# Performance work log

Hardware: AMD Instinct MI355X
Metric: run time of the kernel (lower is better)

## Reference

```python
import jax, jax.numpy as jnp
import numpy as np
import math

V = 32000      # vocab_size
CTX = 1025     # context_length (S = CTX-1)
L = 4          # num_layers
D = 1024       # hidden_dim
H = 16         # heads
DH = D // H    # head_dim
FF = 4 * D
B = 2
PAD = 3        # padding_idx / tokenizer.pad_id()


def setup_inputs() -> dict:
    key = jax.random.key(0)
    ks = jax.random.split(key, 16)
    g = lambda k, shape: jax.random.normal(k, shape, dtype=jnp.float32) * 0.02
    text = jax.random.randint(ks[0], (B, CTX), 0, V)
    emb = g(ks[1], (V, D)).at[PAD].set(0.0)   # nn.Embedding with padding_idx=3
    u = g(ks[2], (H, DH))
    v = g(ks[3], (H, DH))
    Wq = g(ks[4], (L, D, D))
    Wk = g(ks[5], (L, D, D))
    Wv = g(ks[6], (L, D, D))
    Wr = g(ks[7], (L, D, D))
    Wfc = g(ks[8], (L, D, D))
    bfc = jnp.zeros((L, D), jnp.float32)
    ln1g = jnp.ones((L, D), jnp.float32); ln1b = jnp.zeros((L, D), jnp.float32)
    ln2g = jnp.ones((L, D), jnp.float32); ln2b = jnp.zeros((L, D), jnp.float32)
    W1 = g(ks[9], (L, D, FF)); b1 = jnp.zeros((L, FF), jnp.float32)
    W2 = g(ks[10], (L, FF, D)); b2 = jnp.zeros((L, D), jnp.float32)
    lnfg = jnp.ones((D,), jnp.float32); lnfb = jnp.zeros((D,), jnp.float32)
    Wlm = g(ks[11], (D, V)); blm = jnp.zeros((V,), jnp.float32)
    return dict(text=text, emb=emb, u=u, v=v, Wq=Wq, Wk=Wk, Wv=Wv, Wr=Wr,
                Wfc=Wfc, bfc=bfc, ln1g=ln1g, ln1b=ln1b, ln2g=ln2g, ln2b=ln2b,
                W1=W1, b1=b1, W2=W2, b2=b2, lnfg=lnfg, lnfb=lnfb, Wlm=Wlm, blm=blm)


def _ln(x, g, b, eps=1e-5):
    m = x.mean(-1, keepdims=True)
    va = ((x - m) ** 2).mean(-1, keepdims=True)
    return (x - m) / jnp.sqrt(va + eps) * g + b


def _rel_shift(x):
    # Transformer-XL relative shift: pad a zero column, reshape, drop first row.
    b, h, s, r = x.shape
    xp = jnp.pad(x, ((0, 0), (0, 0), (0, 0), (1, 0)))     # (b,h,s,r+1)
    xp = xp.reshape(b, h, r + 1, s)
    return xp[:, :, 1:, :].reshape(b, h, s, r)


def _forward(text, emb, u, v, Wq, Wk, Wv, Wr, Wfc, bfc, ln1g, ln1b, ln2g, ln2b,
             W1, b1, W2, b2, lnfg, lnfb, Wlm, blm):
    ip = text[:, :-1]                 # ip_text = text[:, :-1]
    S = ip.shape[1]
    x = emb[ip]                       # (B,S,D)
    # PositionalEmbedding over Transformer-XL positions [S-1 .. 0]
    pos = jnp.arange(S - 1, -1, -1, dtype=jnp.float32)
    inv_freq = 1.0 / (10000.0 ** (jnp.arange(0, D, 2, dtype=jnp.float32) / D))
    sinu = pos[:, None] * inv_freq[None, :]
    rel = jnp.concatenate([jnp.sin(sinu), jnp.cos(sinu)], axis=-1)  # (S,D)
    # get_mask: causal triu OR pad-token rows
    causal = jnp.triu(jnp.ones((S, S), dtype=bool), 1)
    pad = (ip == PAD)
    mask = (pad[:, :, None] | causal[None]) [:, None, :, :]        # (B,1,S,S)
    full_row = mask.all(-1, keepdims=True)                          # fully-masked rows -> NaN-fill 0
    scale = 1.0 / math.sqrt(DH)
    for l in range(L):
        xn = _ln(x, ln1g[l], ln1b[l])
        q = (xn @ Wq[l]).reshape(B, S, H, DH).transpose(0, 2, 1, 3)   # (B,H,S,DH)
        k = (xn @ Wk[l]).reshape(B, S, H, DH).transpose(0, 2, 1, 3)
        vv = (xn @ Wv[l]).reshape(B, S, H, DH).transpose(0, 2, 1, 3)
        r = (rel @ Wr[l]).reshape(S, H, DH).transpose(1, 0, 2)        # (H,S,DH)
        term_AC = jnp.einsum('bhqd,bhkd->bhqk', q + u[None, :, None, :], k)
        term_BD = jnp.einsum('bhqd,hkd->bhqk', q + v[None, :, None, :], r)
        term_BD = _rel_shift(term_BD)
        scores = (term_AC + term_BD) * scale
        scores = jnp.where(mask, -1e30, scores)
        aw = jax.nn.softmax(scores, axis=-1)
        aw = jnp.where(full_row, 0.0, aw)                              # NaN -> 0 masking
        o = jnp.einsum('bhqk,bhkd->bhqd', aw, vv).transpose(0, 2, 1, 3).reshape(B, S, D)
        o = o @ Wfc[l] + bfc[l] + xn                                   # fc(out) + attn-input residual
        x = x + o                                                      # block residual
        h = _ln(x, ln2g[l], ln2b[l])
        f = jax.nn.gelu(h @ W1[l] + b1[l])
        f = jax.nn.gelu(f @ W2[l] + b2[l])
        x = x + f
    xf = _ln(x, lnfg, lnfb)
    return xf @ Wlm + blm                                              # (B,S,V) logits


def reference(text, emb, u, v, Wq, Wk, Wv, Wr, Wfc, bfc, ln1g, ln1b, ln2g, ln2b,
              W1, b1, W2, b2, lnfg, lnfb, Wlm, blm):
    return _forward(text, emb, u, v, Wq, Wk, Wv, Wr, Wfc, bfc, ln1g, ln1b,
                    ln2g, ln2b, W1, b1, W2, b2, lnfg, lnfb, Wlm, blm)
```

## Files before the change

### kernel.cpp

```cpp
#include <hip/hip_runtime.h>
#include <stdint.h>

#define S_ 1024
#define D_ 1024
#define H_ 16
#define DH_ 64
#define FF_ 4096
#define B_ 2
#define V_ 32000
#define CTX_ 1025
#define PAD_ 3

typedef unsigned short u16;
typedef __attribute__((ext_vector_type(8))) short bf16x8;
typedef __attribute__((ext_vector_type(4))) float f32x4;

enum { EPI_BF16 = 0, EPI_QKV = 1, EPI_FC = 2, EPI_GELU_BF16 = 3, EPI_GELU_RES = 4, EPI_BIAS_F32 = 5 };

__device__ __forceinline__ u16 f2bf(float f) {
  unsigned u = __float_as_uint(f);
  return (u16)((u + 0x7FFFu + ((u >> 16) & 1u)) >> 16);
}

__device__ __forceinline__ float gelu_f(float x) {
  float t = tanhf(0.7978845608028654f * (x + 0.044715f * x * x * x));
  return 0.5f * x * (1.0f + t);
}

__device__ __forceinline__ void glds16(const void* g, void* l) {
  __builtin_amdgcn_global_load_lds(
      (const __attribute__((address_space(1))) unsigned int*)g,
      (__attribute__((address_space(3))) unsigned int*)l,
      16, 0, 0);
}

__global__ __launch_bounds__(256) void embed_gather(const int* __restrict__ text,
                                                    const float* __restrict__ emb,
                                                    float* __restrict__ x) {
  int row = blockIdx.x;
  int b = row >> 10, s = row & 1023;
  int id = text[b * CTX_ + s];
  float4 v = ((const float4*)(emb + (size_t)id * D_))[threadIdx.x];
  ((float4*)(x + (size_t)row * D_))[threadIdx.x] = v;
}

__global__ __launch_bounds__(256) void rel_enc(u16* __restrict__ rel) {
  int i = blockIdx.x;
  float pos = (float)(S_ - 1 - i);
  for (int t = threadIdx.x; t < 512; t += 256) {
    float invf = exp2f(-(float)t * (13.287712379549449f / 512.0f));
    float ang = pos * invf;
    rel[(size_t)i * D_ + t] = f2bf(sinf(ang));
    rel[(size_t)i * D_ + 512 + t] = f2bf(cosf(ang));
  }
}

__global__ __launch_bounds__(256) void wconv_t(const float* __restrict__ src,
                                               u16* __restrict__ dst, int K, int N) {
  src += (size_t)blockIdx.z * K * N;
  dst += (size_t)blockIdx.z * K * N;
  __shared__ float tile[32][33];
  int n0 = blockIdx.x * 32, k0 = blockIdx.y * 32;
  for (int idx = threadIdx.x; idx < 1024; idx += 256) {
    int r = idx >> 5, c = idx & 31;
    tile[r][c] = src[(size_t)(k0 + r) * N + n0 + c];
  }
  __syncthreads();
  for (int idx = threadIdx.x; idx < 1024; idx += 256) {
    int r = idx >> 5, c = idx & 31;
    dst[(size_t)(n0 + r) * K + k0 + c] = f2bf(tile[c][r]);
  }
}

__global__ __launch_bounds__(256) void wconv4_k(const float* __restrict__ sq,
                                                const float* __restrict__ sk,
                                                const float* __restrict__ sv,
                                                const float* __restrict__ sf,
                                                u16* __restrict__ dqkv,
                                                u16* __restrict__ dfc) {
  const int z = blockIdx.z;
  const float* src = (z == 0) ? sq : (z == 1) ? sk : (z == 2) ? sv : sf;
  u16* dst = (z < 3) ? dqkv + (size_t)z * 1024 * 1024 : dfc;
  __shared__ float tile[32][33];
  int n0 = blockIdx.x * 32, k0 = blockIdx.y * 32;
  for (int idx = threadIdx.x; idx < 1024; idx += 256) {
    int r = idx >> 5, c = idx & 31;
    tile[r][c] = src[(size_t)(k0 + r) * 1024 + n0 + c];
  }
  __syncthreads();
  for (int idx = threadIdx.x; idx < 1024; idx += 256) {
    int r = idx >> 5, c = idx & 31;
    dst[(size_t)(n0 + r) * 1024 + k0 + c] = f2bf(tile[c][r]);
  }
}

__global__ __launch_bounds__(256) void layernorm_k(const float* __restrict__ x,
                                                   const float* __restrict__ g,
                                                   const float* __restrict__ bb,
                                                   float* __restrict__ outf,
                                                   u16* __restrict__ outb) {
  int row = blockIdx.x, tid = threadIdx.x;
  const float* xr = x + (size_t)row * D_;
  float4 v = ((const float4*)xr)[tid];
  float s = v.x + v.y + v.z + v.w;
  float s2 = v.x * v.x + v.y * v.y + v.z * v.z + v.w * v.w;
  __shared__ float red[8];
#pragma unroll
  for (int off = 32; off > 0; off >>= 1) { s += __shfl_xor(s, off); s2 += __shfl_xor(s2, off); }
  if ((tid & 63) == 0) { red[tid >> 6] = s; red[4 + (tid >> 6)] = s2; }
  __syncthreads();
  s = red[0] + red[1] + red[2] + red[3];
  s2 = red[4] + red[5] + red[6] + red[7];
  float mean = s * (1.0f / D_);
  float var = s2 * (1.0f / D_) - mean * mean;
  float rstd = rsqrtf(var + 1e-5f);
  float4 gv = ((const float4*)g)[tid];
  float4 bv = ((const float4*)bb)[tid];
  float y0 = (v.x - mean) * rstd * gv.x + bv.x;
  float y1 = (v.y - mean) * rstd * gv.y + bv.y;
  float y2 = (v.z - mean) * rstd * gv.z + bv.z;
  float y3 = (v.w - mean) * rstd * gv.w + bv.w;
  if (outf) ((float4*)(outf + (size_t)row * D_))[tid] = make_float4(y0, y1, y2, y3);
  ((ushort4*)(outb + (size_t)row * D_))[tid] = make_ushort4(f2bf(y0), f2bf(y1), f2bf(y2), f2bf(y3));
}

__device__ __forceinline__ void epi_one(int mode, float v, int row, int col, int ldc,
                                        void* C0p, void* C1p, void* C2p, void* C3p,
                                        const float* bias0, const float* bias1,
                                        const float* res0) {
  if (mode == EPI_QKV) {
    int seg = col >> 10, c = col & 1023;
    size_t idx = (size_t)row * 1024 + c;
    if (seg == 0) {
      ((u16*)C0p)[idx] = f2bf(v + bias0[c]);
      ((u16*)C1p)[idx] = f2bf(v + bias1[c]);
    } else if (seg == 1) {
      ((u16*)C2p)[idx] = f2bf(v);
    } else {
      ((u16*)C3p)[idx] = f2bf(v);
    }
    return;
  }
  size_t idx = (size_t)row * ldc + col;
  float b0 = bias0 ? bias0[col] : 0.0f;
  if (mode == EPI_BF16) {
    ((u16*)C0p)[idx] = f2bf(v);
  } else if (mode == EPI_FC) {
    float* C0 = (float*)C0p;
    C0[idx] = C0[idx] + v + b0 + res0[idx];
  } else if (mode == EPI_GELU_BF16) {
    ((u16*)C0p)[idx] = f2bf(gelu_f(v + b0));
  } else if (mode == EPI_GELU_RES) {
    float* C0 = (float*)C0p;
    C0[idx] = C0[idx] + gelu_f(v + b0);
  } else {
    ((float*)C0p)[idx] = v + b0;
  }
}

__global__ __launch_bounds__(256) void gemm_bt(const u16* __restrict__ A,
                                               const u16* __restrict__ Bt,
                                               int M, int N, int K,
                                               void* __restrict__ C0p, void* __restrict__ C1p,
                                               void* __restrict__ C2p, void* __restrict__ C3p,
                                               const float* __restrict__ bias0,
                                               const float* __restrict__ bias1,
                                               const float* __restrict__ res0,
                                               int ldc, int mode) {
  __shared__ u16 lA[128 * 32];
  __shared__ u16 lB[128 * 32];
  const int tid = threadIdx.x;
  const int wave = tid >> 6, lane = tid & 63;
  const int i0 = blockIdx.y * 128, j0 = blockIdx.x * 128;
  const int wm = wave & 1, wn = wave >> 1;
  const int m_lane = lane & 15, quad = lane >> 4;

  f32x4 acc[4][4] = {};

  const u16* Ab = A + (size_t)i0 * K;
  const u16* Bb = Bt + (size_t)j0 * K;
  const int r0 = wave * 32 + (lane >> 2);
  const int cb = (lane & 3) * 8;

  for (int k0 = 0; k0 < K; k0 += 32) {
    glds16(Ab + (size_t)r0 * K + k0 + cb, lA + wave * 1024);
    glds16(Ab + (size_t)(r0 + 16) * K + k0 + cb, lA + wave * 1024 + 512);
    glds16(Bb + (size_t)r0 * K + k0 + cb, lB + wave * 1024);
    glds16(Bb + (size_t)(r0 + 16) * K + k0 + cb, lB + wave * 1024 + 512);
    __syncthreads();
    bf16x8 af[4], bfr[4];
#pragma unroll
    for (int t = 0; t < 4; t++) {
      af[t] = *(const bf16x8*)(lA + (wm * 64 + t * 16 + m_lane) * 32 + quad * 8);
      bfr[t] = *(const bf16x8*)(lB + (wn * 64 + t * 16 + m_lane) * 32 + quad * 8);
    }
#pragma unroll
    for (int mt = 0; mt < 4; mt++)
#pragma unroll
      for (int nt = 0; nt < 4; nt++)
        acc[mt][nt] = __builtin_amdgcn_mfma_f32_16x16x32_bf16(af[mt], bfr[nt], acc[mt][nt], 0, 0, 0);
    __syncthreads();
  }

#pragma unroll
  for (int mt = 0; mt < 4; mt++) {
#pragma unroll
    for (int nt = 0; nt < 4; nt++) {
      int col = j0 + wn * 64 + nt * 16 + m_lane;
#pragma unroll
      for (int r = 0; r < 4; r++) {
        int row = i0 + wm * 64 + mt * 16 + quad * 4 + r;
        epi_one(mode, acc[mt][nt][r], row, col, ldc, C0p, C1p, C2p, C3p, bias0, bias1, res0);
      }
    }
  }
}

__global__ __launch_bounds__(256) void gemm_bt64(const u16* __restrict__ A,
                                                 const u16* __restrict__ Bt,
                                                 int M, int N, int K,
                                                 void* __restrict__ C0p, void* __restrict__ C1p,
                                                 void* __restrict__ C2p, void* __restrict__ C3p,
                                                 const float* __restrict__ bias0,
                                                 const float* __restrict__ bias1,
                                                 const float* __restrict__ res0,
                                                 int ldc, int mode) {
  __shared__ u16 lA[64 * 32];
  __shared__ u16 lB[128 * 32];
  const int tid = threadIdx.x;
  const int wave = tid >> 6, lane = tid & 63;
  const int i0 = blockIdx.y * 64, j0 = blockIdx.x * 128;
  const int m_lane = lane & 15, quad = lane >> 4;

  f32x4 acc[4][2] = {};

  const u16* Ab = A + (size_t)i0 * K;
  const u16* Bb = Bt + (size_t)j0 * K;
  const int rA = wave * 16 + (lane >> 2);
  const int rB = wave * 32 + (lane >> 2);
  const int cb = (lane & 3) * 8;

  for (int k0 = 0; k0 < K; k0 += 32) {
    glds16(Ab + (size_t)rA * K + k0 + cb, lA + wave * 512);
    glds16(Bb + (size_t)rB * K + k0 + cb, lB + wave * 1024);
    glds16(Bb + (size_t)(rB + 16) * K + k0 + cb, lB + wave * 1024 + 512);
    __syncthreads();
    bf16x8 af[4], bfr[2];
#pragma unroll
    for (int t = 0; t < 4; t++)
      af[t] = *(const bf16x8*)(lA + (t * 16 + m_lane) * 32 + quad * 8);
#pragma unroll
    for (int t = 0; t < 2; t++)
      bfr[t] = *(const bf16x8*)(lB + (wave * 32 + t * 16 + m_lane) * 32 + quad * 8);
#pragma unroll
    for (int mt = 0; mt < 4; mt++)
#pragma unroll
      for (int nt = 0; nt < 2; nt++)
        acc[mt][nt] = __builtin_amdgcn_mfma_f32_16x16x32_bf16(af[mt], bfr[nt], acc[mt][nt], 0, 0, 0);
    __syncthreads();
  }

#pragma unroll
  for (int mt = 0; mt < 4; mt++) {
#pragma unroll
    for (int nt = 0; nt < 2; nt++) {
      int col = j0 + wave * 32 + nt * 16 + m_lane;
#pragma unroll
      for (int r = 0; r < 4; r++) {
        int row = i0 + mt * 16 + quad * 4 + r;
        epi_one(mode, acc[mt][nt][r], row, col, ldc, C0p, C1p, C2p, C3p, bias0, bias1, res0);
      }
    }
  }
}

__global__ __launch_bounds__(256) void attn_gemm(const u16* __restrict__ A, int lda,
                                                 const u16* __restrict__ Bt, int ldb,
                                                 float* __restrict__ Cf, u16* __restrict__ Cb,
                                                 int K, int mode) {
  const int ti = blockIdx.x, tj = blockIdx.y, bh = blockIdx.z;
  if (mode == 0 && tj > ti) return;
  if (mode == 1 && ti + tj < 15) return;
  const int b = bh >> 4, h = bh & 15;
  __shared__ u16 lA[64 * 64];
  __shared__ u16 lB[64 * 64];
  const int tid = threadIdx.x, wave = tid >> 6, lane = tid & 63;
  const int m_lane = lane & 15, quad = lane >> 4;
  const int i0 = ti * 64, j0 = tj * 64;

  size_t aoff, boff;
  if (mode == 0)      { aoff = (size_t)b * S_ * D_ + h * DH_; boff = (size_t)b * S_ * D_ + h * DH_; }
  else if (mode == 1) { aoff = (size_t)b * S_ * D_ + h * DH_; boff = (size_t)h * DH_; }
  else                { aoff = (size_t)bh * S_ * S_;          boff = (size_t)bh * DH_ * S_; }
  const u16* Ap = A + aoff + (size_t)i0 * lda;
  const u16* Bp = Bt + boff + (mode == 2 ? (size_t)0 : (size_t)j0 * ldb);

  f32x4 acc[4] = {};
  const int cid0 = wave * 128 + lane, cid1 = cid0 + 64;
  const int ar0 = cid0 >> 3, ac0 = (cid0 & 7) * 8;
  const int ar1 = cid1 >> 3, ac1 = (cid1 & 7) * 8;

  const int Kend = (mode == 2) ? (ti + 1) * 64 : K;
  for (int k0 = 0; k0 < Kend; k0 += 64) {
    glds16(Ap + (size_t)ar0 * lda + k0 + ac0, lA + wave * 1024);
    glds16(Ap + (size_t)ar1 * lda + k0 + ac1, lA + wave * 1024 + 512);
    glds16(Bp + (size_t)ar0 * ldb + k0 + ac0, lB + wave * 1024);
    glds16(Bp + (size_t)ar1 * ldb + k0 + ac1, lB + wave * 1024 + 512);
    __syncthreads();
    bf16x8 a0 = *(const bf16x8*)(lA + (wave * 16 + m_lane) * 64 + quad * 8);
    bf16x8 a1 = *(const bf16x8*)(lA + (wave * 16 + m_lane) * 64 + 32 + quad * 8);
#pragma unroll
    for (int nt = 0; nt < 4; nt++) {
      bf16x8 b0 = *(const bf16x8*)(lB + (nt * 16 + m_lane) * 64 + quad * 8);
      bf16x8 b1 = *(const bf16x8*)(lB + (nt * 16 + m_lane) * 64 + 32 + quad * 8);
      acc[nt] = __builtin_amdgcn_mfma_f32_16x16x32_bf16(a0, b0, acc[nt], 0, 0, 0);
      acc[nt] = __builtin_amdgcn_mfma_f32_16x16x32_bf16(a1, b1, acc[nt], 0, 0, 0);
    }
    __syncthreads();
  }

  if (mode == 0) {
    float* C = Cf + (size_t)bh * S_ * S_;
#pragma unroll
    for (int nt = 0; nt < 4; nt++) {
      int col = j0 + nt * 16 + m_lane;
#pragma unroll
      for (int r = 0; r < 4; r++) {
        int row = i0 + wave * 16 + quad * 4 + r;
        C[(size_t)row * S_ + col] = acc[nt][r];
      }
    }
  } else if (mode == 1) {
    float* C = Cf + (size_t)bh * S_ * S_;
#pragma unroll
    for (int nt = 0; nt < 4; nt++) {
      int t = j0 + nt * 16 + m_lane;
#pragma unroll
      for (int r = 0; r < 4; r++) {
        int row = i0 + wave * 16 + quad * 4 + r;
        int j = row + t - (S_ - 1);
        if (j >= 0) C[(size_t)row * S_ + j] += acc[nt][r];
      }
    }
  } else {
    u16* C = Cb + (size_t)b * S_ * D_ + h * DH_;
#pragma unroll
    for (int nt = 0; nt < 4; nt++) {
      int col = nt * 16 + m_lane;
#pragma unroll
      for (int r = 0; r < 4; r++) {
        int row = i0 + wave * 16 + quad * 4 + r;
        C[(size_t)row * D_ + col] = f2bf(acc[nt][r]);
      }
    }
  }
}

__global__ __launch_bounds__(256) void softmax_k(const float* __restrict__ scores,
                                                 u16* __restrict__ aw,
                                                 const int* __restrict__ text) {
  const int i = blockIdx.x, bh = blockIdx.y, b = bh >> 4;
  const float* s = scores + ((size_t)bh * S_ + i) * S_;
  u16* o = aw + ((size_t)bh * S_ + i) * S_;
  const int tid = threadIdx.x, wave = tid >> 6, lane = tid & 63;
  const int n = i + 1;
  const int jmax = ((i >> 6) + 1) << 6;
  const int j0 = tid * 4;
  if (text[b * CTX_ + i] == PAD_) {
    if (j0 < jmax) ((ushort4*)o)[tid] = make_ushort4(0, 0, 0, 0);
    return;
  }
  const float scale = 0.125f;
  float4 sv = ((const float4*)s)[tid];
  float e0 = (j0 + 0 < n) ? sv.x * scale : -3e38f;
  float e1 = (j0 + 1 < n) ? sv.y * scale : -3e38f;
  float e2 = (j0 + 2 < n) ? sv.z * scale : -3e38f;
  float e3 = (j0 + 3 < n) ? sv.w * scale : -3e38f;
  float mx = fmaxf(fmaxf(e0, e1), fmaxf(e2, e3));
  __shared__ float red[8];
#pragma unroll
  for (int off = 32; off > 0; off >>= 1) mx = fmaxf(mx, __shfl_xor(mx, off));
  if (lane == 0) red[wave] = mx;
  __syncthreads();
  mx = fmaxf(fmaxf(red[0], red[1]), fmaxf(red[2], red[3]));
  float p0 = __expf(e0 - mx);
  float p1 = __expf(e1 - mx);
  float p2 = __expf(e2 - mx);
  float p3 = __expf(e3 - mx);
  float sum = p0 + p1 + p2 + p3;
#pragma unroll
  for (int off = 32; off > 0; off >>= 1) sum += __shfl_xor(sum, off);
  if (lane == 0) red[4 + wave] = sum;
  __syncthreads();
  sum = red[4] + red[5] + red[6] + red[7];
  float inv = 1.0f / sum;
  if (j0 < jmax)
    ((ushort4*)o)[tid] = make_ushort4(f2bf(p0 * inv), f2bf(p1 * inv), f2bf(p2 * inv), f2bf(p3 * inv));
}

__global__ __launch_bounds__(256) void v_transpose(const u16* __restrict__ v,
                                                   u16* __restrict__ vT) {
  int bh = blockIdx.y, b = bh >> 4, h = bh & 15;
  int j0 = blockIdx.x * 64;
  __shared__ u16 tile[64][65];
  for (int idx = threadIdx.x; idx < 4096; idx += 256) {
    int jj = idx >> 6, d = idx & 63;
    tile[jj][d] = v[(size_t)(b * S_ + j0 + jj) * D_ + h * DH_ + d];
  }
  __syncthreads();
  for (int idx = threadIdx.x; idx < 4096; idx += 256) {
    int d = idx >> 6, jj = idx & 63;
    vT[((size_t)bh * DH_ + d) * S_ + j0 + jj] = tile[jj][d];
  }
}

extern "C" void kernel_launch(void* const* d_in, const int* in_sizes, int n_in,
                              void* d_out, int out_size, void* d_ws, size_t ws_size,
                              hipStream_t stream) {
  (void)in_sizes; (void)n_in; (void)out_size;
  const int* text = (const int*)d_in[0];
  const float* emb = (const float*)d_in[1];
  const float* u_in = (const float*)d_in[2];
  const float* v_in = (const float*)d_in[3];
  const float* Wq = (const float*)d_in[4];
  const float* Wk = (const float*)d_in[5];
  const float* Wv = (const float*)d_in[6];
  const float* Wr = (const float*)d_in[7];
  const float* Wfc = (const float*)d_in[8];
  const float* bfc = (const float*)d_in[9];
  const float* ln1g = (const float*)d_in[10];
  const float* ln1b = (const float*)d_in[11];
  const float* ln2g = (const float*)d_in[12];
  const float* ln2b = (const float*)d_in[13];
  const float* W1 = (const float*)d_in[14];
  const float* b1 = (const float*)d_in[15];
  const float* W2 = (const float*)d_in[16];
  const float* b2 = (const float*)d_in[17];
  const float* lnfg = (const float*)d_in[18];
  const float* lnfb = (const float*)d_in[19];
  const float* Wlm = (const float*)d_in[20];
  const float* blm = (const float*)d_in[21];
  float* out = (float*)d_out;

  char* w = (char*)d_ws;
  size_t off = 0;
  auto alloc = [&](size_t bytes) -> void* {
    void* p = w + off;
    off += (bytes + 255) & ~(size_t)255;
    return p;
  };
  float* x      = (float*)alloc(2048ull * 1024 * 4);
  float* xnf    = (float*)alloc(2048ull * 1024 * 4);
  u16* xnb      = (u16*)alloc(2048ull * 1024 * 2);
  u16* relb     = (u16*)alloc(1024ull * 1024 * 2);
  u16* wqkvt    = (u16*)alloc(3072ull * 1024 * 2);
  u16* wrt_all  = (u16*)alloc(4096ull * 1024 * 2);
  u16* wfct     = (u16*)alloc(1024ull * 1024 * 2);
  u16* w1t      = (u16*)alloc(4096ull * 1024 * 2);
  u16* w2t      = (u16*)alloc(4096ull * 1024 * 2);
  u16* wlmt     = (u16*)alloc(32000ull * 1024 * 2);
  u16* qu       = (u16*)alloc(2048ull * 1024 * 2);
  u16* qv       = (u16*)alloc(2048ull * 1024 * 2);
  u16* kk       = (u16*)alloc(2048ull * 1024 * 2);
  u16* vv       = (u16*)alloc(2048ull * 1024 * 2);
  u16* vT       = (u16*)alloc(2048ull * 1024 * 2);
  u16* rb_all   = (u16*)alloc(1024ull * 4096 * 2);
  float* scores = (float*)alloc(32ull * 1024 * 1024 * 4);
  u16* aw       = (u16*)alloc(32ull * 1024 * 1024 * 2);
  u16* o_       = (u16*)alloc(2048ull * 1024 * 2);
  u16* f1       = (u16*)alloc(2048ull * 4096 * 2);
  if (off > ws_size) return;

  dim3 blk(256);
  embed_gather<<<2048, blk, 0, stream>>>(text, emb, x);
  rel_enc<<<1024, blk, 0, stream>>>(relb);
  wconv_t<<<dim3(1000, 32), blk, 0, stream>>>(Wlm, wlmt, 1024, 32000);
  wconv_t<<<dim3(32, 32, 4), blk, 0, stream>>>(Wr, wrt_all, 1024, 1024);
  gemm_bt<<<dim3(32, 8), blk, 0, stream>>>(relb, wrt_all, 1024, 4096, 1024,
                                           rb_all, nullptr, nullptr, nullptr,
                                           nullptr, nullptr, nullptr, 4096, EPI_BF16);

  for (int l = 0; l < 4; l++) {
    const size_t dd = 1048576;
    wconv4_k<<<dim3(32, 32, 4), blk, 0, stream>>>(Wq + l * dd, Wk + l * dd, Wv + l * dd,
                                                  Wfc + l * dd, wqkvt, wfct);
    wconv_t<<<dim3(128, 32), blk, 0, stream>>>(W1 + l * 4ull * dd, w1t, 1024, 4096);
    wconv_t<<<dim3(32, 128), blk, 0, stream>>>(W2 + l * 4ull * dd, w2t, 4096, 1024);

    layernorm_k<<<2048, blk, 0, stream>>>(x, ln1g + l * 1024, ln1b + l * 1024, xnf, xnb);

    gemm_bt<<<dim3(24, 16), blk, 0, stream>>>(xnb, wqkvt, 2048, 3072, 1024,
                                              qu, qv, kk, vv, u_in, v_in, nullptr, 1024, EPI_QKV);
    v_transpose<<<dim3(16, 32), blk, 0, stream>>>(vv, vT);

    attn_gemm<<<dim3(16, 16, 32), blk, 0, stream>>>(qu, 1024, kk, 1024, scores, nullptr, 64, 0);
    attn_gemm<<<dim3(16, 16, 32), blk, 0, stream>>>(qv, 1024, rb_all + (size_t)l * 1024, 4096,
                                                    scores, nullptr, 64, 1);
    softmax_k<<<dim3(1024, 32), blk, 0, stream>>>(scores, aw, text);
    attn_gemm<<<dim3(16, 1, 32), blk, 0, stream>>>(aw, 1024, vT, 1024, nullptr, o_, 1024, 2);

    gemm_bt64<<<dim3(8, 32), blk, 0, stream>>>(o_, wfct, 2048, 1024, 1024,
                                               x, nullptr, nullptr, nullptr,
                                               bfc + l * 1024, nullptr, xnf, 1024, EPI_FC);
    layernorm_k<<<2048, blk, 0, stream>>>(x, ln2g + l * 1024, ln2b + l * 1024, nullptr, xnb);
    gemm_bt<<<dim3(32, 16), blk, 0, stream>>>(xnb, w1t, 2048, 4096, 1024,
                                              f1, nullptr, nullptr, nullptr,
                                              b1 + l * 4096, nullptr, nullptr, 4096, EPI_GELU_BF16);
    gemm_bt64<<<dim3(8, 32), blk, 0, stream>>>(f1, w2t, 2048, 1024, 4096,
                                               x, nullptr, nullptr, nullptr,
                                               b2 + l * 1024, nullptr, nullptr, 1024, EPI_GELU_RES);
  }

  layernorm_k<<<2048, blk, 0, stream>>>(x, lnfg, lnfb, nullptr, xnb);
  gemm_bt<<<dim3(250, 16), blk, 0, stream>>>(xnb, wlmt, 2048, 32000, 1024,
                                             out, nullptr, nullptr, nullptr,
                                             blm, nullptr, nullptr, 32000, EPI_BIAS_F32);
}
```

Measured before the change: 2.420 ms.

## Fuse AC and BD score GEMMs with in-block relative shift over causal tiles

Replaces the two separate attention score launches, the content term and the position term with a later read-modify-write, by one kernel. That kernel launches only the 136 lower-triangular tiles per head, computes both terms in registers, and applies the relative shift through a shared-memory staging of the two needed position tiles. It also adds an XCD-aware workgroup remapping to both GEMM kernels and makes softmax skip loading score entries above the causal block. The fused kernel rounds the position term to bf16 before adding it and reads operands straight from global memory without LDS tiling. Both choices risk some precision and load efficiency.

Measured after the change: 2.349 ms. 3.0% less time.

```diff
diff --git a/kernel.cpp b/kernel.cpp
--- a/kernel.cpp
+++ b/kernel.cpp
@@ -20,6 +20,10 @@
 __device__ __forceinline__ u16 f2bf(float f) {
   unsigned u = __float_as_uint(f);
   return (u16)((u + 0x7FFFu + ((u >> 16) & 1u)) >> 16);
+}
+
+__device__ __forceinline__ float bf2f(u16 v) {
+  return __uint_as_float(((unsigned)v) << 16);
 }
 
 __device__ __forceinline__ float gelu_f(float x) {
@@ -171,7 +175,16 @@
   __shared__ u16 lB[128 * 32];
   const int tid = threadIdx.x;
   const int wave = tid >> 6, lane = tid & 63;
-  const int i0 = blockIdx.y * 128, j0 = blockIdx.x * 128;
+  unsigned gx = gridDim.x, gy = gridDim.y;
+  unsigned nwg = gx * gy;
+  unsigned bx = blockIdx.x, by = blockIdx.y;
+  if ((nwg & 7u) == 0u) {
+    unsigned lin = by * gx + bx;
+    unsigned v = (lin & 7u) * (nwg >> 3) + (lin >> 3);
+    bx = v / gy;
+    by = v - bx * gy;
+  }
+  const int i0 = by * 128, j0 = bx * 128;
   const int wm = wave & 1, wn = wave >> 1;
   const int m_lane = lane & 15, quad = lane >> 4;
 
@@ -229,7 +242,16 @@
   __shared__ u16 lB[128 * 32];
   const int tid = threadIdx.x;
   const int wave = tid >> 6, lane = tid & 63;
-  const int i0 = blockIdx.y * 64, j0 = blockIdx.x * 128;
+  unsigned gx = gridDim.x, gy = gridDim.y;
+  unsigned nwg = gx * gy;
+  unsigned bx = blockIdx.x, by = blockIdx.y;
+  if ((nwg & 7u) == 0u) {
+    unsigned lin = by * gx + bx;
+    unsigned v = (lin & 7u) * (nwg >> 3) + (lin >> 3);
+    by = v / gx;
+    bx = v - by * gx;
+  }
+  const int i0 = by * 64, j0 = bx * 128;
   const int m_lane = lane & 15, quad = lane >> 4;
 
   f32x4 acc[4][2] = {};
@@ -270,6 +292,82 @@
         int row = i0 + mt * 16 + quad * 4 + r;
         epi_one(mode, acc[mt][nt][r], row, col, ldc, C0p, C1p, C2p, C3p, bias0, bias1, res0);
       }
+    }
+  }
+}
+
+__global__ __launch_bounds__(256) void attn_score(const u16* __restrict__ qu,
+                                                  const u16* __restrict__ qv,
+                                                  const u16* __restrict__ kk,
+                                                  const u16* __restrict__ rb,
+                                                  float* __restrict__ scores) {
+  __shared__ u16 sBD[64][132];
+  const int cIdx = blockIdx.x, bh = blockIdx.y;
+  int ti = (int)((sqrtf(8.0f * (float)cIdx + 1.0f) - 1.0f) * 0.5f);
+  while ((ti + 1) * (ti + 2) / 2 <= cIdx) ti++;
+  while (ti * (ti + 1) / 2 > cIdx) ti--;
+  const int tj = cIdx - ti * (ti + 1) / 2;
+  const int b = bh >> 4, h = bh & 15;
+  const int tid = threadIdx.x, wave = tid >> 6, lane = tid & 63;
+  const int m_lane = lane & 15, quad = lane >> 4;
+  const int i0 = ti * 64, j0 = tj * 64;
+  const int T0 = 15 - (ti - tj);
+  const bool hasT1 = (T0 < 15);
+
+  const u16* Qu = qu + ((size_t)(b * S_ + i0 + wave * 16 + m_lane)) * D_ + h * DH_ + quad * 8;
+  const u16* Qv = qv + ((size_t)(b * S_ + i0 + wave * 16 + m_lane)) * D_ + h * DH_ + quad * 8;
+  bf16x8 a0 = *(const bf16x8*)(Qu);
+  bf16x8 a1 = *(const bf16x8*)(Qu + 32);
+  bf16x8 c0 = *(const bf16x8*)(Qv);
+  bf16x8 c1 = *(const bf16x8*)(Qv + 32);
+
+  const u16* Kb = kk + ((size_t)(b * S_ + j0)) * D_ + h * DH_;
+  const u16* R0 = rb + ((size_t)(T0 * 64)) * 4096 + h * DH_;
+  const u16* R1 = R0 + (size_t)64 * 4096;
+
+  f32x4 ac_[4] = {}, bd0_[4] = {}, bd1_[4] = {};
+#pragma unroll
+  for (int nt = 0; nt < 4; nt++) {
+    const u16* kr = Kb + (size_t)(nt * 16 + m_lane) * D_ + quad * 8;
+    bf16x8 kb0 = *(const bf16x8*)(kr);
+    bf16x8 kb1 = *(const bf16x8*)(kr + 32);
+    ac_[nt] = __builtin_amdgcn_mfma_f32_16x16x32_bf16(a0, kb0, ac_[nt], 0, 0, 0);
+    ac_[nt] = __builtin_amdgcn_mfma_f32_16x16x32_bf16(a1, kb1, ac_[nt], 0, 0, 0);
+    const u16* rr = R0 + (size_t)(nt * 16 + m_lane) * 4096 + quad * 8;
+    bf16x8 rb0 = *(const bf16x8*)(rr);
+    bf16x8 rb1 = *(const bf16x8*)(rr + 32);
+    bd0_[nt] = __builtin_amdgcn_mfma_f32_16x16x32_bf16(c0, rb0, bd0_[nt], 0, 0, 0);
+    bd0_[nt] = __builtin_amdgcn_mfma_f32_16x16x32_bf16(c1, rb1, bd0_[nt], 0, 0, 0);
+    if (hasT1) {
+      const u16* r2 = R1 + (size_t)(nt * 16 + m_lane) * 4096 + quad * 8;
+      bf16x8 rc0 = *(const bf16x8*)(r2);
+      bf16x8 rc1 = *(const bf16x8*)(r2 + 32);
+      bd1_[nt] = __builtin_amdgcn_mfma_f32_16x16x32_bf16(c0, rc0, bd1_[nt], 0, 0, 0);
+      bd1_[nt] = __builtin_amdgcn_mfma_f32_16x16x32_bf16(c1, rc1, bd1_[nt], 0, 0, 0);
+    }
+  }
+
+#pragma unroll
+  for (int nt = 0; nt < 4; nt++) {
+    int col = nt * 16 + m_lane;
+#pragma unroll
+    for (int r = 0; r < 4; r++) {
+      int row = wave * 16 + quad * 4 + r;
+      sBD[row][col] = f2bf(bd0_[nt][r]);
+      sBD[row][64 + col] = hasT1 ? f2bf(bd1_[nt][r]) : (u16)0;
+    }
+  }
+  __syncthreads();
+
+  float* C = scores + (size_t)bh * S_ * S_ + (size_t)i0 * S_ + j0;
+#pragma unroll
+  for (int nt = 0; nt < 4; nt++) {
+    int jl = nt * 16 + m_lane;
+#pragma unroll
+    for (int r = 0; r < 4; r++) {
+      int il = wave * 16 + quad * 4 + r;
+      int tloc = jl - il + 63;
+      C[(size_t)il * S_ + jl] = ac_[nt][r] + bf2f(sBD[il][tloc]);
     }
   }
 }
@@ -371,7 +469,8 @@
     return;
   }
   const float scale = 0.125f;
-  float4 sv = ((const float4*)s)[tid];
+  float4 sv = make_float4(0.f, 0.f, 0.f, 0.f);
+  if (j0 < jmax) sv = ((const float4*)s)[tid];
   float e0 = (j0 + 0 < n) ? sv.x * scale : -3e38f;
   float e1 = (j0 + 1 < n) ? sv.y * scale : -3e38f;
   float e2 = (j0 + 2 < n) ? sv.z * scale : -3e38f;
@@ -493,9 +592,7 @@
                                               qu, qv, kk, vv, u_in, v_in, nullptr, 1024, EPI_QKV);
     v_transpose<<<dim3(16, 32), blk, 0, stream>>>(vv, vT);
 
-    attn_gemm<<<dim3(16, 16, 32), blk, 0, stream>>>(qu, 1024, kk, 1024, scores, nullptr, 64, 0);
-    attn_gemm<<<dim3(16, 16, 32), blk, 0, stream>>>(qv, 1024, rb_all + (size_t)l * 1024, 4096,
-                                                    scores, nullptr, 64, 1);
+    attn_score<<<dim3(136, 32), blk, 0, stream>>>(qu, qv, kk, rb_all + (size_t)l * 1024, scores);
     softmax_k<<<dim3(1024, 32), blk, 0, stream>>>(scores, aw, text);
     attn_gemm<<<dim3(16, 1, 32), blk, 0, stream>>>(aw, 1024, vT, 1024, nullptr, o_, 1024, 2);
 
```
